# Kernel optimization log

Measured on AMD Instinct MI355X. Metric: run time of the kernel, lower is better.

Reference implementation:

```python
import jax, jax.numpy as jnp
import numpy as np

FEATURE_SIZE = 1_000_000
FIELD_SIZE = 39
DIM = 16
BATCH = 8192
CROSS = FIELD_SIZE * (FIELD_SIZE - 1) // 2  # 741


def _pair_index():
    # [[i, j] for i in range(F-1) for j in range(i+1, F)] -> [CROSS, 2]
    idx = [[i, j] for i in range(FIELD_SIZE - 1) for j in range(i + 1, FIELD_SIZE)]
    return jnp.asarray(np.array(idx, dtype=np.int32))


def setup_inputs() -> dict:
    key = jax.random.key(0)
    k1, k2, k3, k4 = jax.random.split(key, 4)
    inputs = jax.random.randint(k1, (BATCH, FIELD_SIZE), 0, FEATURE_SIZE, dtype=jnp.int32)
    embedding_weights = jax.random.normal(k2, (FEATURE_SIZE, DIM), dtype=jnp.float32) * 0.05
    field_weights = jax.random.normal(k3, (CROSS, 1), dtype=jnp.float32) * 0.1
    linear_weights = jax.random.normal(k4, (FEATURE_SIZE,), dtype=jnp.float32) * 0.05
    bias_weight = jnp.zeros((), dtype=jnp.float32)
    return {
        "inputs": inputs,
        "embedding_weights": embedding_weights,
        "field_weights": field_weights,
        "linear_weights": linear_weights,
        "bias_weight": bias_weight,
    }


def reference(inputs, embedding_weights, field_weights, linear_weights, bias_weight):
    pair_idx = _pair_index()  # [CROSS, 2]

    # first order: sum of linear weights over fields -> [B, 1]
    first_order = jnp.sum(linear_weights[inputs], axis=1, keepdims=True)
    bias = jnp.ones_like(first_order) * bias_weight

    # gather each field's embedding once, then index the pairs (same math as
    # the double gather in the original, avoids re-gathering the big table)
    field_emb = embedding_weights[inputs]            # [B, F, D]
    e_i = field_emb[:, pair_idx[:, 0], :]            # [B, CROSS, D]
    e_j = field_emb[:, pair_idx[:, 1], :]            # [B, CROSS, D]
    second_items = jnp.sum(e_i * e_j, axis=-1)       # [B, CROSS]
    second_order = second_items @ field_weights      # [B, 1]

    return bias + first_order + second_order
```

## Files before the change

### kernel.cpp

```cpp
#include <hip/hip_runtime.h>
#include <utility>

#define FIELD 39
#define DIM 16
#define CROSS 741
#define BATCH 8192

__host__ __device__ constexpr int pair_base(int i) {
    return i * (FIELD - 1) - i * (i - 1) / 2;
}


template <size_t... Fs>
__device__ __forceinline__ void gather_row(const int* __restrict__ rowIdx,
                                           const float* __restrict__ emb,
                                           int d, float (&e)[FIELD],
                                           std::index_sequence<Fs...>) {
    int idx[FIELD];
    ((idx[Fs] = rowIdx[Fs]), ...);
    ((e[Fs] = emb[(size_t)idx[Fs] * DIM + d]), ...);
}

template <int I, size_t... Js>
__device__ __forceinline__ float row_inner(const float (&e)[FIELD],
                                           const float* __restrict__ fw,
                                           std::index_sequence<Js...>) {
    float s = 0.f;
    ((s = fmaf(fw[pair_base(I) + (int)Js], e[I + 1 + (int)Js], s)), ...);
    return s;
}

template <size_t... Is>
__device__ __forceinline__ float pair_sum(const float (&e)[FIELD],
                                          const float* __restrict__ fw,
                                          std::index_sequence<Is...>) {
    float acc[4] = {0.f, 0.f, 0.f, 0.f};
    ((acc[Is & 3] = fmaf(e[Is],
                         row_inner<(int)Is>(e, fw, std::make_index_sequence<FIELD - 1 - Is>{}),
                         acc[Is & 3])),
     ...);
    return (acc[0] + acc[1]) + (acc[2] + acc[3]);
}

__global__ __launch_bounds__(256) void fwfm_kernel(
    const int*   __restrict__ inputs,
    const float* __restrict__ emb,
    const float* __restrict__ fw,
    const float* __restrict__ lw,
    const float* __restrict__ bias,
    float*       __restrict__ out)
{
    const int tid  = threadIdx.x;
    const int lane = tid & 63;
    const int wave = tid >> 6;
    const int d    = lane & 15;
    const int rloc = lane >> 4;
    const int row  = blockIdx.x * 16 + wave * 4 + rloc;

    const int* rowIdx = inputs + row * FIELD;

    float e[FIELD];
    gather_row(rowIdx, emb, d, e, std::make_index_sequence<FIELD>{});

    float fo = lw[rowIdx[d]] + lw[rowIdx[d + 16]];
    if (d + 32 < FIELD) fo += lw[rowIdx[d + 32]];

    float acc = pair_sum(e, fw, std::make_index_sequence<FIELD - 1>{});

    float tot = fo + acc;
    tot += __shfl_xor(tot, 1, 64);
    tot += __shfl_xor(tot, 2, 64);
    tot += __shfl_xor(tot, 4, 64);
    tot += __shfl_xor(tot, 8, 64);

    if (d == 0) out[row] = tot + bias[0];
}

extern "C" void kernel_launch(void* const* d_in, const int* in_sizes, int n_in,
                              void* d_out, int out_size, void* d_ws, size_t ws_size,
                              hipStream_t stream) {
    const int*   inputs = (const int*)  d_in[0];
    const float* emb    = (const float*)d_in[1];
    const float* fw     = (const float*)d_in[2];
    const float* lw     = (const float*)d_in[3];
    const float* bias   = (const float*)d_in[4];
    float*       out    = (float*)      d_out;

    dim3 grid(BATCH / 16);
    fwfm_kernel<<<grid, 256, 0, stream>>>(inputs, emb, fw, lw, bias, out);
}
```

Before: 112.3 us.

## Tile field embeddings into 13-field blocks to cut live registers

Instead of holding all 39 gathered embedding values in registers at once, the kernel loads three tiles of 13 fields and computes the pairwise sum block by block: diagonal blocks plus off-diagonal blocks. Tile 1 is reloaded from global memory so that only two tiles are live at a time. This is meant to lower register pressure and raise occupancy, which helps hide the latency of the random gathers. The cost is extra gather traffic for the reloaded tile and a gather/compute order that is more serialized.

```diff
diff --git a/kernel.cpp b/kernel.cpp
--- a/kernel.cpp
+++ b/kernel.cpp
@@ -2,44 +2,67 @@
 #include <utility>
 
 #define FIELD 39
-#define DIM 16
-#define CROSS 741
+#define TILE  13
+#define DIM   16
 #define BATCH 8192
 
 __host__ __device__ constexpr int pair_base(int i) {
     return i * (FIELD - 1) - i * (i - 1) / 2;
 }
-
-
-template <size_t... Fs>
-__device__ __forceinline__ void gather_row(const int* __restrict__ rowIdx,
-                                           const float* __restrict__ emb,
-                                           int d, float (&e)[FIELD],
-                                           std::index_sequence<Fs...>) {
-    int idx[FIELD];
-    ((idx[Fs] = rowIdx[Fs]), ...);
-    ((e[Fs] = emb[(size_t)idx[Fs] * DIM + d]), ...);
+__host__ __device__ constexpr int widx(int i, int j) {
+    return pair_base(i) + (j - i - 1);
 }
 
-template <int I, size_t... Js>
-__device__ __forceinline__ float row_inner(const float (&e)[FIELD],
+template <int T, size_t... Ks>
+__device__ __forceinline__ void load_tile(const int* __restrict__ rowIdx,
+                                          const float* __restrict__ emb,
+                                          int d, float (&e)[TILE],
+                                          std::index_sequence<Ks...>) {
+    int idx[TILE];
+    ((idx[Ks] = rowIdx[T * TILE + (int)Ks]), ...);
+    ((e[Ks] = emb[(size_t)idx[Ks] * DIM + d]), ...);
+}
+
+template <int A, int B, int II, size_t... Js>
+__device__ __forceinline__ float inner_off(const float (&eB)[TILE],
                                            const float* __restrict__ fw,
                                            std::index_sequence<Js...>) {
     float s = 0.f;
-    ((s = fmaf(fw[pair_base(I) + (int)Js], e[I + 1 + (int)Js], s)), ...);
+    ((s = fmaf(fw[widx(A * TILE + II, B * TILE + (int)Js)], eB[Js], s)), ...);
     return s;
 }
-
-template <size_t... Is>
-__device__ __forceinline__ float pair_sum(const float (&e)[FIELD],
+template <int A, int B, size_t... Is>
+__device__ __forceinline__ void block_off(const float (&eA)[TILE],
+                                          const float (&eB)[TILE],
                                           const float* __restrict__ fw,
+                                          float (&acc)[4],
                                           std::index_sequence<Is...>) {
-    float acc[4] = {0.f, 0.f, 0.f, 0.f};
-    ((acc[Is & 3] = fmaf(e[Is],
-                         row_inner<(int)Is>(e, fw, std::make_index_sequence<FIELD - 1 - Is>{}),
+    ((acc[Is & 3] = fmaf(eA[Is],
+                         inner_off<A, B, (int)Is>(eB, fw, std::make_index_sequence<TILE>{}),
                          acc[Is & 3])),
      ...);
-    return (acc[0] + acc[1]) + (acc[2] + acc[3]);
+}
+
+template <int A, int II, size_t... Js>
+__device__ __forceinline__ float inner_diag(const float (&e)[TILE],
+                                            const float* __restrict__ fw,
+                                            std::index_sequence<Js...>) {
+    float s = 0.f;
+    ((s = fmaf(fw[widx(A * TILE + II, A * TILE + II + 1 + (int)Js)],
+               e[II + 1 + Js], s)),
+     ...);
+    return s;
+}
+template <int A, size_t... Is>
+__device__ __forceinline__ void block_diag(const float (&e)[TILE],
+                                           const float* __restrict__ fw,
+                                           float (&acc)[4],
+                                           std::index_sequence<Is...>) {
+    ((acc[Is & 3] = fmaf(e[Is],
+                         inner_diag<A, (int)Is>(e, fw,
+                             std::make_index_sequence<TILE - 1 - Is>{}),
+                         acc[Is & 3])),
+     ...);
 }
 
 __global__ __launch_bounds__(256) void fwfm_kernel(
@@ -59,15 +82,26 @@
 
     const int* rowIdx = inputs + row * FIELD;
 
-    float e[FIELD];
-    gather_row(rowIdx, emb, d, e, std::make_index_sequence<FIELD>{});
+    float fo = lw[rowIdx[d]] + lw[rowIdx[d + 16]];
+    if (d < 7) fo += lw[rowIdx[d + 32]];
 
-    float fo = lw[rowIdx[d]] + lw[rowIdx[d + 16]];
-    if (d + 32 < FIELD) fo += lw[rowIdx[d + 32]];
+    float eA[TILE], eB[TILE];
+    float acc[4] = {0.f, 0.f, 0.f, 0.f};
+    const auto seqT = std::make_index_sequence<TILE>{};
 
-    float acc = pair_sum(e, fw, std::make_index_sequence<FIELD - 1>{});
+    load_tile<0>(rowIdx, emb, d, eA, seqT);
+    block_diag<0>(eA, fw, acc, seqT);
+    load_tile<1>(rowIdx, emb, d, eB, seqT);
+    block_off<0, 1>(eA, eB, fw, acc, seqT);
+    load_tile<2>(rowIdx, emb, d, eB, seqT);
+    block_off<0, 2>(eA, eB, fw, acc, seqT);
+    load_tile<1>(rowIdx, emb, d, eA, seqT);
+    block_diag<1>(eA, fw, acc, seqT);
+    block_off<1, 2>(eA, eB, fw, acc, seqT);
+    block_diag<2>(eB, fw, acc, seqT);
+    float so = (acc[0] + acc[1]) + (acc[2] + acc[3]);
 
-    float tot = fo + acc;
+    float tot = fo + so;
     tot += __shfl_xor(tot, 1, 64);
     tot += __shfl_xor(tot, 2, 64);
     tot += __shfl_xor(tot, 4, 64);
```

New measurement: 108.1 us. -3.7%, faster.

## Stage field weights in LDS as padded tiled layout and read via float4

Applied to the files above, without the earlier changes.

Field-pair weights are remapped at compile time into a tiled, zero-padded layout (three 13-field tiles, with off-diagonal and diagonal blocks) and copied into shared memory once per block. The pairwise loop then reads them with 16-byte LDS loads instead of many scalar global loads. It also adds a launch-bounds occupancy hint. The cost is an extra staging loop with a __syncthreads per block, a few wasted FMAs on padding, and a larger embedding register array that may raise register pressure.

```diff
diff --git a/kernel.cpp b/kernel.cpp
--- a/kernel.cpp
+++ b/kernel.cpp
@@ -2,47 +2,82 @@
 #include <utility>
 
 #define FIELD 39
-#define DIM 16
-#define CROSS 741
+#define TILE  13
+#define DIM   16
 #define BATCH 8192
+#define EPAD  42
 
-__host__ __device__ constexpr int pair_base(int i) {
-    return i * (FIELD - 1) - i * (i - 1) / 2;
+constexpr int widx(int i, int j) { return i*(FIELD-1) - i*(i-1)/2 + (j-i-1); }
+constexpr int ceil4(int x) { return (x+3) & ~3; }
+constexpr int OFF_ROW  = 16;
+constexpr int OFF_TILE = TILE * OFF_ROW;
+constexpr int diag_rowstart(int II) {
+    int s = 0; for (int m = 0; m < II; ++m) s += ceil4(TILE-1-m); return s;
 }
+constexpr int DIAG_TILE = diag_rowstart(TILE);
+constexpr int off_base(int t) { return t * OFF_TILE; }
+constexpr int diag_base(int A) { return 3*OFF_TILE + A*DIAG_TILE; }
+constexpr int WTOT = 3*OFF_TILE + 3*DIAG_TILE;
 
+struct WMap { int v[WTOT]; };
+constexpr WMap make_map() {
+    WMap m{};
+    for (int i = 0; i < WTOT; ++i) m.v[i] = -1;
+    const int AB[3][2] = {{0,1},{0,2},{1,2}};
+    for (int t = 0; t < 3; ++t)
+        for (int II = 0; II < TILE; ++II)
+            for (int c = 0; c < TILE; ++c)
+                m.v[off_base(t) + II*OFF_ROW + c] = widx(AB[t][0]*TILE+II, AB[t][1]*TILE+c);
+    for (int A = 0; A < 3; ++A)
+        for (int II = 0; II < TILE-1; ++II)
+            for (int k = 0; k < TILE-1-II; ++k)
+                m.v[diag_base(A) + diag_rowstart(II) + k] = widx(A*TILE+II, A*TILE+II+1+k);
+    return m;
+}
+__device__ constexpr WMap g_map = make_map();
 
+__device__ __forceinline__ float4 ld4(const float* lds, int ofs) {
+    return *reinterpret_cast<const float4*>(lds + ofs);
+}
+template <int EB>
+__device__ __forceinline__ float fma4(float4 w, const float (&e)[EPAD], float s) {
+    s = fmaf(w.x, e[EB+0], s); s = fmaf(w.y, e[EB+1], s);
+    s = fmaf(w.z, e[EB+2], s); s = fmaf(w.w, e[EB+3], s);
+    return s;
+}
+template <int RBASE, int EBASE, size_t... Qs>
+__device__ __forceinline__ float row_q(const float* lds, const float (&e)[EPAD],
+                                       std::index_sequence<Qs...>) {
+    float s = 0.f;
+    ((s = fma4<EBASE + 4*(int)Qs>(ld4(lds, RBASE + 4*(int)Qs), e, s)), ...);
+    return s;
+}
+template <int T, int A, int B, size_t... IIs>
+__device__ __forceinline__ void block_off(const float* lds, const float (&e)[EPAD],
+                                          float (&acc)[4], std::index_sequence<IIs...>) {
+    ((acc[IIs & 3] = fmaf(e[A*TILE + (int)IIs],
+         row_q<off_base(T) + (int)IIs*OFF_ROW, B*TILE>(lds, e, std::make_index_sequence<4>{}),
+         acc[IIs & 3])), ...);
+}
+template <int A, size_t... IIs>
+__device__ __forceinline__ void block_diag(const float* lds, const float (&e)[EPAD],
+                                           float (&acc)[4], std::index_sequence<IIs...>) {
+    ((acc[IIs & 3] = fmaf(e[A*TILE + (int)IIs],
+         row_q<diag_base(A) + diag_rowstart((int)IIs), A*TILE + (int)IIs + 1>(
+             lds, e, std::make_index_sequence<(size_t)(ceil4(TILE-1-(int)IIs)/4)>{}),
+         acc[IIs & 3])), ...);
+}
 template <size_t... Fs>
-__device__ __forceinline__ void gather_row(const int* __restrict__ rowIdx,
+__device__ __forceinline__ void gather_all(const int* __restrict__ rowIdx,
                                            const float* __restrict__ emb,
-                                           int d, float (&e)[FIELD],
+                                           int d, float (&e)[EPAD],
                                            std::index_sequence<Fs...>) {
     int idx[FIELD];
     ((idx[Fs] = rowIdx[Fs]), ...);
     ((e[Fs] = emb[(size_t)idx[Fs] * DIM + d]), ...);
 }
 
-template <int I, size_t... Js>
-__device__ __forceinline__ float row_inner(const float (&e)[FIELD],
-                                           const float* __restrict__ fw,
-                                           std::index_sequence<Js...>) {
-    float s = 0.f;
-    ((s = fmaf(fw[pair_base(I) + (int)Js], e[I + 1 + (int)Js], s)), ...);
-    return s;
-}
-
-template <size_t... Is>
-__device__ __forceinline__ float pair_sum(const float (&e)[FIELD],
-                                          const float* __restrict__ fw,
-                                          std::index_sequence<Is...>) {
-    float acc[4] = {0.f, 0.f, 0.f, 0.f};
-    ((acc[Is & 3] = fmaf(e[Is],
-                         row_inner<(int)Is>(e, fw, std::make_index_sequence<FIELD - 1 - Is>{}),
-                         acc[Is & 3])),
-     ...);
-    return (acc[0] + acc[1]) + (acc[2] + acc[3]);
-}
-
-__global__ __launch_bounds__(256) void fwfm_kernel(
+__global__ __launch_bounds__(256, 2) void fwfm_kernel(
     const int*   __restrict__ inputs,
     const float* __restrict__ emb,
     const float* __restrict__ fw,
@@ -50,6 +85,8 @@
     const float* __restrict__ bias,
     float*       __restrict__ out)
 {
+    __shared__ __align__(16) float wlds[WTOT];
+
     const int tid  = threadIdx.x;
     const int lane = tid & 63;
     const int wave = tid >> 6;
@@ -59,15 +96,30 @@
 
     const int* rowIdx = inputs + row * FIELD;
 
-    float e[FIELD];
-    gather_row(rowIdx, emb, d, e, std::make_index_sequence<FIELD>{});
+    float e[EPAD];
+    gather_all(rowIdx, emb, d, e, std::make_index_sequence<FIELD>{});
+    e[39] = 0.f; e[40] = 0.f; e[41] = 0.f;
+
+    for (int s = tid; s < WTOT; s += 256) {
+        int m = g_map.v[s];
+        wlds[s] = (m >= 0) ? fw[m] : 0.f;
+    }
+    __syncthreads();
 
     float fo = lw[rowIdx[d]] + lw[rowIdx[d + 16]];
-    if (d + 32 < FIELD) fo += lw[rowIdx[d + 32]];
+    if (d < 7) fo += lw[rowIdx[d + 32]];
 
-    float acc = pair_sum(e, fw, std::make_index_sequence<FIELD - 1>{});
+    float acc[4] = {0.f, 0.f, 0.f, 0.f};
+    const auto seqT = std::make_index_sequence<TILE>{};
+    block_off<0, 0, 1>(wlds, e, acc, seqT);
+    block_off<1, 0, 2>(wlds, e, acc, seqT);
+    block_off<2, 1, 2>(wlds, e, acc, seqT);
+    block_diag<0>(wlds, e, acc, seqT);
+    block_diag<1>(wlds, e, acc, seqT);
+    block_diag<2>(wlds, e, acc, seqT);
+    float so = (acc[0] + acc[1]) + (acc[2] + acc[3]);
 
-    float tot = fo + acc;
+    float tot = fo + so;
     tot += __shfl_xor(tot, 1, 64);
     tot += __shfl_xor(tot, 2, 64);
     tot += __shfl_xor(tot, 4, 64);
```

Measured after the change: 108.3 us. 3.5% less time.
